# Kernel tuning notes

Measured on AMD Instinct MI355X. Metric: run time of the kernel, lower is better.

## Reference

```python
import jax, jax.numpy as jnp
import numpy as np

EPS = 1e-08
ORDINAL = 2.0

def setup_inputs() -> dict:
    key = jax.random.key(0)
    k1, k2, k3, k4, k5 = jax.random.split(key, 5)
    B, IN, OUT = 1024, 256, 1024
    inputs = jax.random.normal(k1, (B, IN), dtype=jnp.float32)
    weights = jax.random.normal(k2, (OUT, IN), dtype=jnp.float32) * (1.0 / np.sqrt(IN))
    biases = jax.random.normal(k3, (OUT,), dtype=jnp.float32) * (1.0 / np.sqrt(IN))
    centers = jax.random.normal(k4, (OUT, IN), dtype=jnp.float32) * 0.1
    # diag inv covars ~ U(3/(IN+0.5), 3/(IN-0.5)) per reset_parameters
    inv_covars = jax.random.uniform(k5, (OUT, IN), dtype=jnp.float32,
                                    minval=3.0 / (IN + 0.5), maxval=3.0 / (IN - 0.5))
    return {"inputs": inputs, "weights": weights, "biases": biases,
            "centers": centers, "inv_covars": inv_covars}

def reference(inputs, weights, biases, centers, inv_covars):
    # linear part: [B, OUT]
    l = inputs @ weights.T + biases
    # diag covar path (ordinal = 2.0, so the 1e-32 stabilizer is absent and
    # pow(c^2, 1/ordinal) == |c| after clamping):
    # g[b, z] = sum_i ( |x[b,i] - c[z,i]| * sqrt(clamp(ic[z,i])^2) )^2
    ic = jnp.minimum(inv_covars, 1.0 / EPS)
    scale = jnp.power(ic * ic, 1.0 / ORDINAL)  # [OUT, IN]
    diff = jnp.abs(inputs[:, None, :] - centers[None, :, :]) * scale[None, :, :]  # [B, OUT, IN]
    g = jnp.exp(-jnp.sum(jnp.power(diff, ORDINAL), axis=-1))  # [B, OUT]
    res = l * g
    return (res, g)
```

## Files before the change

kernel.cpp:

```cpp
#include <hip/hip_runtime.h>
#include <hip/hip_bf16.h>
#include <math.h>


typedef __attribute__((ext_vector_type(8))) short short8;
typedef __attribute__((ext_vector_type(4))) float floatx4;

#define MFMA __builtin_amdgcn_mfma_f32_16x16x32_bf16
#define INDIM 256
#define OUTD  1024
#define BD    1024
#define TM 32
#define TN 32
#define TK 64
#define KSTR 72

__device__ __forceinline__ unsigned pkbf(float a, float b) {
    union { __hip_bfloat162 h; unsigned u; } v;
    v.h = __float22bfloat162_rn(make_float2(a, b));
    return v.u;
}

__global__ __launch_bounds__(256)
void fgn_fused(const float* __restrict__ X, const float* __restrict__ W,
               const float* __restrict__ Bias, const float* __restrict__ C,
               const float* __restrict__ IC, float* __restrict__ Out)
{
    __shared__ __align__(16) unsigned short As [TM * KSTR];
    __shared__ __align__(16) unsigned short As2[TM * KSTR];
    __shared__ __align__(16) unsigned short Bw [TN * KSTR];
    __shared__ __align__(16) unsigned short Bg1[TN * KSTR];
    __shared__ __align__(16) unsigned short Bg2[TN * KSTR];
    __shared__ float sCz[TN];

    const int b    = blockIdx.x;
    const int xcd  = b & 7;
    const int n0   = (xcd + 8 * ((b >> 3) & 3)) * TN;
    const int m0   = (b >> 5) * TM;

    const int t    = threadIdx.x;
    const int w    = t >> 6;
    const int lane = t & 63;
    const int r    = lane & 15;
    const int q    = lane >> 4;
    const int mt   = w & 1;
    const int nt   = w >> 1;

    const int srow = t >> 3;
    const int sk   = (t & 7) << 3;

    floatx4 zero = {0.f, 0.f, 0.f, 0.f};
    floatx4 accL = zero;
    floatx4 accG = zero;
    float czp = 0.f;

    for (int k0 = 0; k0 < INDIM; k0 += TK) {
        const float4* xp = (const float4*)&X[(size_t)(m0 + srow) * INDIM + k0 + sk];
        float4 x0 = xp[0], x1 = xp[1];
        const size_t bo = (size_t)(n0 + srow) * INDIM + k0 + sk;
        const float4* wp = (const float4*)&W[bo];
        const float4* cp = (const float4*)&C[bo];
        const float4* ip = (const float4*)&IC[bo];
        float4 w0 = wp[0], w1 = wp[1];
        float4 c0 = cp[0], c1 = cp[1];
        float4 i0 = ip[0], i1 = ip[1];

        __syncthreads();

        {
            float xf[8] = {x0.x,x0.y,x0.z,x0.w, x1.x,x1.y,x1.z,x1.w};
            uint4* pa  = (uint4*)&As [srow * KSTR + sk];
            uint4* pa2 = (uint4*)&As2[srow * KSTR + sk];
            pa[0]  = make_uint4(pkbf(xf[0],xf[1]), pkbf(xf[2],xf[3]),
                                pkbf(xf[4],xf[5]), pkbf(xf[6],xf[7]));
            pa2[0] = make_uint4(pkbf(xf[0]*xf[0],xf[1]*xf[1]), pkbf(xf[2]*xf[2],xf[3]*xf[3]),
                                pkbf(xf[4]*xf[4],xf[5]*xf[5]), pkbf(xf[6]*xf[6],xf[7]*xf[7]));
        }
        {
            float wf[8] = {w0.x,w0.y,w0.z,w0.w, w1.x,w1.y,w1.z,w1.w};
            float cf[8] = {c0.x,c0.y,c0.z,c0.w, c1.x,c1.y,c1.z,c1.w};
            float ff[8] = {i0.x,i0.y,i0.z,i0.w, i1.x,i1.y,i1.z,i1.w};
            float g1[8], g2[8];
            #pragma unroll
            for (int e = 0; e < 8; ++e) {
                float s  = fminf(ff[e], 1e8f);
                float qq = s * s;
                g2[e] = qq;
                g1[e] = -2.f * cf[e] * qq;
                czp  = fmaf(cf[e] * cf[e], qq, czp);
            }
            const int bb = srow * KSTR + sk;
            *(uint4*)&Bw [bb] = make_uint4(pkbf(wf[0],wf[1]), pkbf(wf[2],wf[3]),
                                           pkbf(wf[4],wf[5]), pkbf(wf[6],wf[7]));
            *(uint4*)&Bg1[bb] = make_uint4(pkbf(g1[0],g1[1]), pkbf(g1[2],g1[3]),
                                           pkbf(g1[4],g1[5]), pkbf(g1[6],g1[7]));
            *(uint4*)&Bg2[bb] = make_uint4(pkbf(g2[0],g2[1]), pkbf(g2[2],g2[3]),
                                           pkbf(g2[4],g2[5]), pkbf(g2[6],g2[7]));
        }
        if (k0 + TK >= INDIM) {
            czp += __shfl_down(czp, 4);
            czp += __shfl_down(czp, 2);
            czp += __shfl_down(czp, 1);
            if ((t & 7) == 0) sCz[srow] = czp;
        }
        __syncthreads();

        #pragma unroll
        for (int kk = 0; kk < 2; ++kk) {
            const int ko = kk * 32 + q * 8;
            short8 a0  = *(const short8*)&As [(mt * 16 + r) * KSTR + ko];
            short8 a2  = *(const short8*)&As2[(mt * 16 + r) * KSTR + ko];
            const int br = (nt * 16 + r) * KSTR + ko;
            short8 bwf = *(const short8*)&Bw [br];
            short8 b1f = *(const short8*)&Bg1[br];
            short8 b2f = *(const short8*)&Bg2[br];
            accL = MFMA(a0, bwf, accL, 0, 0, 0);
            accG = MFMA(a0, b1f, accG, 0, 0, 0);
            accG = MFMA(a2, b2f, accG, 0, 0, 0);
        }
    }

    float* OutR = Out;
    float* OutG = Out + (size_t)BD * OUTD;
    const int n      = n0 + nt * 16 + r;
    const float bias = Bias[n];
    const float cz   = sCz[nt * 16 + r];
    #pragma unroll
    for (int reg = 0; reg < 4; ++reg) {
        const int m = m0 + mt * 16 + q * 4 + reg;
        const float g   = expf(-(accG[reg] + cz));
        const float res = (accL[reg] + bias) * g;
        OutR[(size_t)m * OUTD + n] = res;
        OutG[(size_t)m * OUTD + n] = g;
    }
}

extern "C" void kernel_launch(void* const* d_in, const int* in_sizes, int n_in,
                              void* d_out, int out_size, void* d_ws, size_t ws_size,
                              hipStream_t stream) {
    const float* X    = (const float*)d_in[0];
    const float* W    = (const float*)d_in[1];
    const float* Bias = (const float*)d_in[2];
    const float* C    = (const float*)d_in[3];
    const float* IC   = (const float*)d_in[4];
    float* Out = (float*)d_out;

    fgn_fused<<<1024, 256, 0, stream>>>(X, W, Bias, C, IC, Out);
}
```

Baseline: 71.22 us.

## Split preprocessing into prep kernel and double-buffer bf16 tiles via direct global-to-LDS loads

A separate prep kernel now converts X, X², W and the Gaussian factors to bf16 and precomputes the per-output constant term once, instead of every tile block redoing that conversion. The main kernel streams those bf16 operands straight into XOR-swizzled LDS with global_load_lds, double-buffered so the next K tile loads while the current one computes. It also uses 64-row M tiles with 512 threads. The cost is a second kernel launch, a workspace round trip, and less occupancy from the larger blocks.

```diff
diff --git a/kernel.cpp b/kernel.cpp
--- a/kernel.cpp
+++ b/kernel.cpp
@@ -7,13 +7,10 @@
 typedef __attribute__((ext_vector_type(4))) float floatx4;
 
 #define MFMA __builtin_amdgcn_mfma_f32_16x16x32_bf16
-#define INDIM 256
-#define OUTD  1024
-#define BD    1024
-#define TM 32
-#define TN 32
-#define TK 64
-#define KSTR 72
+
+#define GLDS16(g, l) __builtin_amdgcn_global_load_lds(                      \
+    (const __attribute__((address_space(1))) void*)(g),                     \
+    (__attribute__((address_space(3))) void*)(l), 16, 0, 0)
 
 __device__ __forceinline__ unsigned pkbf(float a, float b) {
     union { __hip_bfloat162 h; unsigned u; } v;
@@ -22,116 +19,139 @@
 }
 
 __global__ __launch_bounds__(256)
-void fgn_fused(const float* __restrict__ X, const float* __restrict__ W,
-               const float* __restrict__ Bias, const float* __restrict__ C,
-               const float* __restrict__ IC, float* __restrict__ Out)
+void fgn_prep(const float* __restrict__ X, const float* __restrict__ W,
+              const float* __restrict__ C, const float* __restrict__ IC,
+              unsigned short* __restrict__ XB, unsigned short* __restrict__ X2B,
+              unsigned short* __restrict__ WB, unsigned short* __restrict__ G1,
+              unsigned short* __restrict__ G2, float* __restrict__ CZ)
 {
-    __shared__ __align__(16) unsigned short As [TM * KSTR];
-    __shared__ __align__(16) unsigned short As2[TM * KSTR];
-    __shared__ __align__(16) unsigned short Bw [TN * KSTR];
-    __shared__ __align__(16) unsigned short Bg1[TN * KSTR];
-    __shared__ __align__(16) unsigned short Bg2[TN * KSTR];
-    __shared__ float sCz[TN];
+    const int t = threadIdx.x, w = t >> 6, l = t & 63;
+    const int b = blockIdx.x;
+    if (b < 256) {
+        const int z = b * 4 + w;
+        const int o = z * 256 + l * 4;
+        const float4 c4 = *(const float4*)&C[o];
+        const float4 i4 = *(const float4*)&IC[o];
+        const float4 w4 = *(const float4*)&W[o];
+        float s;
+        s = fminf(i4.x, 1e8f); const float q0 = s * s;
+        s = fminf(i4.y, 1e8f); const float q1 = s * s;
+        s = fminf(i4.z, 1e8f); const float q2 = s * s;
+        s = fminf(i4.w, 1e8f); const float q3 = s * s;
+        float czp = c4.x*c4.x*q0 + c4.y*c4.y*q1 + c4.z*c4.z*q2 + c4.w*c4.w*q3;
+        *(uint2*)&WB[o] = make_uint2(pkbf(w4.x, w4.y), pkbf(w4.z, w4.w));
+        *(uint2*)&G1[o] = make_uint2(pkbf(-2.f*c4.x*q0, -2.f*c4.y*q1),
+                                     pkbf(-2.f*c4.z*q2, -2.f*c4.w*q3));
+        *(uint2*)&G2[o] = make_uint2(pkbf(q0, q1), pkbf(q2, q3));
+        #pragma unroll
+        for (int off = 32; off; off >>= 1) czp += __shfl_down(czp, off);
+        if (l == 0) CZ[z] = czp;
+    } else {
+        const int m = (b - 256) * 4 + w;
+        const int o = m * 256 + l * 4;
+        const float4 x4 = *(const float4*)&X[o];
+        *(uint2*)&XB[o]  = make_uint2(pkbf(x4.x, x4.y), pkbf(x4.z, x4.w));
+        *(uint2*)&X2B[o] = make_uint2(pkbf(x4.x*x4.x, x4.y*x4.y),
+                                      pkbf(x4.z*x4.z, x4.w*x4.w));
+    }
+}
 
-    const int b    = blockIdx.x;
-    const int xcd  = b & 7;
-    const int n0   = (xcd + 8 * ((b >> 3) & 3)) * TN;
-    const int m0   = (b >> 5) * TM;
+#define L_AX   0
+#define L_AX2  8192
+#define L_BW   16384
+#define L_BG1  20480
+#define L_BG2  24576
+#define L_BUF  28672
+
+__global__ __launch_bounds__(512)
+void fgn_main(const unsigned short* __restrict__ XB, const unsigned short* __restrict__ X2B,
+              const unsigned short* __restrict__ WB, const unsigned short* __restrict__ G1,
+              const unsigned short* __restrict__ G2, const float* __restrict__ Bias,
+              const float* __restrict__ CZ, float* __restrict__ Out)
+{
+    __shared__ __align__(16) char lds[2 * L_BUF];
+
+    const int b  = blockIdx.x;
+    const int n0 = ((b & 7) + 8 * ((b >> 3) & 3)) * 32;
+    const int m0 = (b >> 5) * 64;
 
     const int t    = threadIdx.x;
     const int w    = t >> 6;
     const int lane = t & 63;
     const int r    = lane & 15;
     const int q    = lane >> 4;
-    const int mt   = w & 1;
-    const int nt   = w >> 1;
+    const int mt   = w & 3;
+    const int nt   = w >> 2;
 
-    const int srow = t >> 3;
-    const int sk   = (t & 7) << 3;
+    const int rt = t >> 3;
+    const int cs = ((t & 7) << 4) ^ ((rt & 7) << 4);
+    const int srcA = (m0 + rt) * 512 + cs;
+    const int srcB = (n0 + rt) * 512 + cs;
+    const int wbase = (t >> 6) << 10;
 
     floatx4 zero = {0.f, 0.f, 0.f, 0.f};
     floatx4 accL = zero;
     floatx4 accG = zero;
-    float czp = 0.f;
 
-    for (int k0 = 0; k0 < INDIM; k0 += TK) {
-        const float4* xp = (const float4*)&X[(size_t)(m0 + srow) * INDIM + k0 + sk];
-        float4 x0 = xp[0], x1 = xp[1];
-        const size_t bo = (size_t)(n0 + srow) * INDIM + k0 + sk;
-        const float4* wp = (const float4*)&W[bo];
-        const float4* cp = (const float4*)&C[bo];
-        const float4* ip = (const float4*)&IC[bo];
-        float4 w0 = wp[0], w1 = wp[1];
-        float4 c0 = cp[0], c1 = cp[1];
-        float4 i0 = ip[0], i1 = ip[1];
+    auto STAGE = [&](int buf, int k0) {
+        char* L = lds + buf * L_BUF;
+        const int kb = k0 << 1;
+        GLDS16((const char*)XB  + srcA + kb, L + L_AX  + wbase);
+        GLDS16((const char*)X2B + srcA + kb, L + L_AX2 + wbase);
+        if (t < 256) {
+            GLDS16((const char*)WB + srcB + kb, L + L_BW  + wbase);
+            GLDS16((const char*)G1 + srcB + kb, L + L_BG1 + wbase);
+            GLDS16((const char*)G2 + srcB + kb, L + L_BG2 + wbase);
+        }
+    };
 
-        __syncthreads();
-
-        {
-            float xf[8] = {x0.x,x0.y,x0.z,x0.w, x1.x,x1.y,x1.z,x1.w};
-            uint4* pa  = (uint4*)&As [srow * KSTR + sk];
-            uint4* pa2 = (uint4*)&As2[srow * KSTR + sk];
-            pa[0]  = make_uint4(pkbf(xf[0],xf[1]), pkbf(xf[2],xf[3]),
-                                pkbf(xf[4],xf[5]), pkbf(xf[6],xf[7]));
-            pa2[0] = make_uint4(pkbf(xf[0]*xf[0],xf[1]*xf[1]), pkbf(xf[2]*xf[2],xf[3]*xf[3]),
-                                pkbf(xf[4]*xf[4],xf[5]*xf[5]), pkbf(xf[6]*xf[6],xf[7]*xf[7]));
-        }
-        {
-            float wf[8] = {w0.x,w0.y,w0.z,w0.w, w1.x,w1.y,w1.z,w1.w};
-            float cf[8] = {c0.x,c0.y,c0.z,c0.w, c1.x,c1.y,c1.z,c1.w};
-            float ff[8] = {i0.x,i0.y,i0.z,i0.w, i1.x,i1.y,i1.z,i1.w};
-            float g1[8], g2[8];
-            #pragma unroll
-            for (int e = 0; e < 8; ++e) {
-                float s  = fminf(ff[e], 1e8f);
-                float qq = s * s;
-                g2[e] = qq;
-                g1[e] = -2.f * cf[e] * qq;
-                czp  = fmaf(cf[e] * cf[e], qq, czp);
-            }
-            const int bb = srow * KSTR + sk;
-            *(uint4*)&Bw [bb] = make_uint4(pkbf(wf[0],wf[1]), pkbf(wf[2],wf[3]),
-                                           pkbf(wf[4],wf[5]), pkbf(wf[6],wf[7]));
-            *(uint4*)&Bg1[bb] = make_uint4(pkbf(g1[0],g1[1]), pkbf(g1[2],g1[3]),
-                                           pkbf(g1[4],g1[5]), pkbf(g1[6],g1[7]));
-            *(uint4*)&Bg2[bb] = make_uint4(pkbf(g2[0],g2[1]), pkbf(g2[2],g2[3]),
-                                           pkbf(g2[4],g2[5]), pkbf(g2[6],g2[7]));
-        }
-        if (k0 + TK >= INDIM) {
-            czp += __shfl_down(czp, 4);
-            czp += __shfl_down(czp, 2);
-            czp += __shfl_down(czp, 1);
-            if ((t & 7) == 0) sCz[srow] = czp;
-        }
-        __syncthreads();
-
+    const int arow = mt * 16 + r;
+    const int brow = nt * 16 + r;
+    auto COMPUTE = [&](int buf) {
+        const char* L = lds + buf * L_BUF;
         #pragma unroll
         for (int kk = 0; kk < 2; ++kk) {
-            const int ko = kk * 32 + q * 8;
-            short8 a0  = *(const short8*)&As [(mt * 16 + r) * KSTR + ko];
-            short8 a2  = *(const short8*)&As2[(mt * 16 + r) * KSTR + ko];
-            const int br = (nt * 16 + r) * KSTR + ko;
-            short8 bwf = *(const short8*)&Bw [br];
-            short8 b1f = *(const short8*)&Bg1[br];
-            short8 b2f = *(const short8*)&Bg2[br];
-            accL = MFMA(a0, bwf, accL, 0, 0, 0);
-            accG = MFMA(a0, b1f, accG, 0, 0, 0);
-            accG = MFMA(a2, b2f, accG, 0, 0, 0);
+            const int ca = kk * 64 + q * 16;
+            const int ao = arow * 128 + (ca ^ ((arow & 7) << 4));
+            const int bo = brow * 128 + (ca ^ ((brow & 7) << 4));
+            short8 a0 = *(const short8*)(L + L_AX  + ao);
+            short8 a2 = *(const short8*)(L + L_AX2 + ao);
+            short8 bw = *(const short8*)(L + L_BW  + bo);
+            short8 b1 = *(const short8*)(L + L_BG1 + bo);
+            short8 b2 = *(const short8*)(L + L_BG2 + bo);
+            accL = MFMA(a0, bw, accL, 0, 0, 0);
+            accG = MFMA(a0, b1, accG, 0, 0, 0);
+            accG = MFMA(a2, b2, accG, 0, 0, 0);
+        }
+    };
+
+    STAGE(0, 0);
+    asm volatile("s_waitcnt vmcnt(0)" ::: "memory");
+    __syncthreads();
+
+    int cur = 0;
+    #pragma unroll
+    for (int k0 = 0; k0 < 256; k0 += 64) {
+        if (k0 + 64 < 256) STAGE(cur ^ 1, k0 + 64);
+        COMPUTE(cur);
+        if (k0 + 64 < 256) {
+            asm volatile("s_waitcnt vmcnt(0)" ::: "memory");
+            __syncthreads();
+            cur ^= 1;
         }
     }
 
-    float* OutR = Out;
-    float* OutG = Out + (size_t)BD * OUTD;
-    const int n      = n0 + nt * 16 + r;
+    const int   n    = n0 + nt * 16 + r;
     const float bias = Bias[n];
-    const float cz   = sCz[nt * 16 + r];
+    const float cz   = CZ[n];
+    float* OutG = Out + (size_t)1024 * 1024;
     #pragma unroll
     for (int reg = 0; reg < 4; ++reg) {
         const int m = m0 + mt * 16 + q * 4 + reg;
         const float g   = expf(-(accG[reg] + cz));
         const float res = (accL[reg] + bias) * g;
-        OutR[(size_t)m * OUTD + n] = res;
-        OutG[(size_t)m * OUTD + n] = g;
+        Out [(size_t)m * 1024 + n] = res;
+        OutG[(size_t)m * 1024 + n] = g;
     }
 }
 
@@ -145,5 +165,13 @@
     const float* IC   = (const float*)d_in[4];
     float* Out = (float*)d_out;
 
-    fgn_fused<<<1024, 256, 0, stream>>>(X, W, Bias, C, IC, Out);
+    unsigned short* XB  = (unsigned short*)d_ws;
+    unsigned short* X2B = XB  + 262144;
+    unsigned short* WB  = X2B + 262144;
+    unsigned short* G1  = WB  + 262144;
+    unsigned short* G2  = G1  + 262144;
+    float*          CZ  = (float*)(G2 + 262144);
+
+    fgn_prep<<<512, 256, 0, stream>>>(X, W, C, IC, XB, X2B, WB, G1, G2, CZ);
+    fgn_main<<<512, 512, 0, stream>>>(XB, X2B, WB, G1, G2, Bias, CZ, Out);
 }
```

New measurement: 70.65 us. About the same (-0.8%).

## Enlarge tiles to 128x32 with 512 threads and prefetch next K slice

Applied to the files above, without the earlier changes.

Each block now covers 128 rows by 32 columns with 512 threads, and each wave computes two 16x16 output tiles. This reuses the B-side operands (W, centers, inverse covariances) across four times as many rows, which cuts redundant global loads and the repeated conversion work on those operands. Half the threads load W while the other half load C and IC. Global loads for the next K slice are issued before the MFMA compute of the current one, so memory latency overlaps with compute. The grid shrinks to 256 blocks, which lowers the number of blocks per CU and drops the previous XCD-aware block mapping.

```diff
diff --git a/kernel.cpp b/kernel.cpp
--- a/kernel.cpp
+++ b/kernel.cpp
@@ -7,12 +7,6 @@
 typedef __attribute__((ext_vector_type(4))) float floatx4;
 
 #define MFMA __builtin_amdgcn_mfma_f32_16x16x32_bf16
-#define INDIM 256
-#define OUTD  1024
-#define BD    1024
-#define TM 32
-#define TN 32
-#define TK 64
 #define KSTR 72
 
 __device__ __forceinline__ unsigned pkbf(float a, float b) {
@@ -21,63 +15,84 @@
     return v.u;
 }
 
-__global__ __launch_bounds__(256)
-void fgn_fused(const float* __restrict__ X, const float* __restrict__ W,
-               const float* __restrict__ Bias, const float* __restrict__ C,
-               const float* __restrict__ IC, float* __restrict__ Out)
+__global__ __launch_bounds__(512)
+void fgn_one(const float* __restrict__ X, const float* __restrict__ W,
+             const float* __restrict__ Bias, const float* __restrict__ C,
+             const float* __restrict__ IC, float* __restrict__ Out)
 {
-    __shared__ __align__(16) unsigned short As [TM * KSTR];
-    __shared__ __align__(16) unsigned short As2[TM * KSTR];
-    __shared__ __align__(16) unsigned short Bw [TN * KSTR];
-    __shared__ __align__(16) unsigned short Bg1[TN * KSTR];
-    __shared__ __align__(16) unsigned short Bg2[TN * KSTR];
-    __shared__ float sCz[TN];
+    __shared__ __align__(16) unsigned short As [128 * KSTR];
+    __shared__ __align__(16) unsigned short As2[128 * KSTR];
+    __shared__ __align__(16) unsigned short Bw [32 * KSTR];
+    __shared__ __align__(16) unsigned short Bg1[32 * KSTR];
+    __shared__ __align__(16) unsigned short Bg2[32 * KSTR];
+    __shared__ float sCz[32];
 
-    const int b    = blockIdx.x;
-    const int xcd  = b & 7;
-    const int n0   = (xcd + 8 * ((b >> 3) & 3)) * TN;
-    const int m0   = (b >> 5) * TM;
+    const int b  = blockIdx.x;
+    const int m0 = (b & 7) * 128;
+    const int n0 = (b >> 3) * 32;
 
     const int t    = threadIdx.x;
     const int w    = t >> 6;
     const int lane = t & 63;
     const int r    = lane & 15;
     const int q    = lane >> 4;
-    const int mt   = w & 1;
-    const int nt   = w >> 1;
+    const int mt   = w & 3;
+    const int nt   = w >> 2;
 
-    const int srow = t >> 3;
-    const int sk   = (t & 7) << 3;
+    const int arow = t >> 3;
+    const int ach  = (t & 7) << 3;
+    const bool isW = (t < 256);
+    const int brow = (t & 255) >> 3;
+
+    float4 xa0, xa1, xb0, xb1;
+    float4 w0, w1, c0, c1, i0, i1;
+    float czp = 0.f;
 
     floatx4 zero = {0.f, 0.f, 0.f, 0.f};
-    floatx4 accL = zero;
-    floatx4 accG = zero;
-    float czp = 0.f;
+    floatx4 accL0 = zero, accL1 = zero, accG0 = zero, accG1 = zero;
 
-    for (int k0 = 0; k0 < INDIM; k0 += TK) {
-        const float4* xp = (const float4*)&X[(size_t)(m0 + srow) * INDIM + k0 + sk];
-        float4 x0 = xp[0], x1 = xp[1];
-        const size_t bo = (size_t)(n0 + srow) * INDIM + k0 + sk;
-        const float4* wp = (const float4*)&W[bo];
-        const float4* cp = (const float4*)&C[bo];
-        const float4* ip = (const float4*)&IC[bo];
-        float4 w0 = wp[0], w1 = wp[1];
-        float4 c0 = cp[0], c1 = cp[1];
-        float4 i0 = ip[0], i1 = ip[1];
+    auto LOADS = [&](int k0) {
+        const float4* p;
+        p = (const float4*)&X[(size_t)(m0 + arow) * 256 + k0 + ach];
+        xa0 = p[0]; xa1 = p[1];
+        p = (const float4*)&X[(size_t)(m0 + arow + 64) * 256 + k0 + ach];
+        xb0 = p[0]; xb1 = p[1];
+        if (isW) {
+            p = (const float4*)&W[(size_t)(n0 + brow) * 256 + k0 + ach];
+            w0 = p[0]; w1 = p[1];
+        } else {
+            p = (const float4*)&C[(size_t)(n0 + brow) * 256 + k0 + ach];
+            c0 = p[0]; c1 = p[1];
+            p = (const float4*)&IC[(size_t)(n0 + brow) * 256 + k0 + ach];
+            i0 = p[0]; i1 = p[1];
+        }
+    };
 
-        __syncthreads();
-
+    auto STORE_LDS = [&](bool last) {
         {
-            float xf[8] = {x0.x,x0.y,x0.z,x0.w, x1.x,x1.y,x1.z,x1.w};
-            uint4* pa  = (uint4*)&As [srow * KSTR + sk];
-            uint4* pa2 = (uint4*)&As2[srow * KSTR + sk];
-            pa[0]  = make_uint4(pkbf(xf[0],xf[1]), pkbf(xf[2],xf[3]),
-                                pkbf(xf[4],xf[5]), pkbf(xf[6],xf[7]));
-            pa2[0] = make_uint4(pkbf(xf[0]*xf[0],xf[1]*xf[1]), pkbf(xf[2]*xf[2],xf[3]*xf[3]),
-                                pkbf(xf[4]*xf[4],xf[5]*xf[5]), pkbf(xf[6]*xf[6],xf[7]*xf[7]));
+            float f0[8] = {xa0.x,xa0.y,xa0.z,xa0.w, xa1.x,xa1.y,xa1.z,xa1.w};
+            float f1[8] = {xb0.x,xb0.y,xb0.z,xb0.w, xb1.x,xb1.y,xb1.z,xb1.w};
+            const int a0 = arow * KSTR + ach;
+            const int a1 = (arow + 64) * KSTR + ach;
+            *(uint4*)&As [a0] = make_uint4(pkbf(f0[0],f0[1]), pkbf(f0[2],f0[3]),
+                                           pkbf(f0[4],f0[5]), pkbf(f0[6],f0[7]));
+            *(uint4*)&As2[a0] = make_uint4(pkbf(f0[0]*f0[0],f0[1]*f0[1]),
+                                           pkbf(f0[2]*f0[2],f0[3]*f0[3]),
+                                           pkbf(f0[4]*f0[4],f0[5]*f0[5]),
+                                           pkbf(f0[6]*f0[6],f0[7]*f0[7]));
+            *(uint4*)&As [a1] = make_uint4(pkbf(f1[0],f1[1]), pkbf(f1[2],f1[3]),
+                                           pkbf(f1[4],f1[5]), pkbf(f1[6],f1[7]));
+            *(uint4*)&As2[a1] = make_uint4(pkbf(f1[0]*f1[0],f1[1]*f1[1]),
+                                           pkbf(f1[2]*f1[2],f1[3]*f1[3]),
+                                           pkbf(f1[4]*f1[4],f1[5]*f1[5]),
+                                           pkbf(f1[6]*f1[6],f1[7]*f1[7]));
         }
-        {
-            float wf[8] = {w0.x,w0.y,w0.z,w0.w, w1.x,w1.y,w1.z,w1.w};
+        const int bb = brow * KSTR + ach;
+        if (isW) {
+            float f[8] = {w0.x,w0.y,w0.z,w0.w, w1.x,w1.y,w1.z,w1.w};
+            *(uint4*)&Bw[bb] = make_uint4(pkbf(f[0],f[1]), pkbf(f[2],f[3]),
+                                          pkbf(f[4],f[5]), pkbf(f[6],f[7]));
+        } else {
             float cf[8] = {c0.x,c0.y,c0.z,c0.w, c1.x,c1.y,c1.z,c1.w};
             float ff[8] = {i0.x,i0.y,i0.z,i0.w, i1.x,i1.y,i1.z,i1.w};
             float g1[8], g2[8];
@@ -89,49 +104,66 @@
                 g1[e] = -2.f * cf[e] * qq;
                 czp  = fmaf(cf[e] * cf[e], qq, czp);
             }
-            const int bb = srow * KSTR + sk;
-            *(uint4*)&Bw [bb] = make_uint4(pkbf(wf[0],wf[1]), pkbf(wf[2],wf[3]),
-                                           pkbf(wf[4],wf[5]), pkbf(wf[6],wf[7]));
             *(uint4*)&Bg1[bb] = make_uint4(pkbf(g1[0],g1[1]), pkbf(g1[2],g1[3]),
                                            pkbf(g1[4],g1[5]), pkbf(g1[6],g1[7]));
             *(uint4*)&Bg2[bb] = make_uint4(pkbf(g2[0],g2[1]), pkbf(g2[2],g2[3]),
                                            pkbf(g2[4],g2[5]), pkbf(g2[6],g2[7]));
+            if (last) {
+                czp += __shfl_down(czp, 4);
+                czp += __shfl_down(czp, 2);
+                czp += __shfl_down(czp, 1);
+                if ((t & 7) == 0) sCz[brow] = czp;
+            }
         }
-        if (k0 + TK >= INDIM) {
-            czp += __shfl_down(czp, 4);
-            czp += __shfl_down(czp, 2);
-            czp += __shfl_down(czp, 1);
-            if ((t & 7) == 0) sCz[srow] = czp;
-        }
-        __syncthreads();
+    };
 
+    const int ar0 = (mt * 32 + r) * KSTR;
+    const int ar1 = ar0 + 16 * KSTR;
+    const int br  = (nt * 16 + r) * KSTR;
+    auto COMPUTE = [&]() {
         #pragma unroll
         for (int kk = 0; kk < 2; ++kk) {
             const int ko = kk * 32 + q * 8;
-            short8 a0  = *(const short8*)&As [(mt * 16 + r) * KSTR + ko];
-            short8 a2  = *(const short8*)&As2[(mt * 16 + r) * KSTR + ko];
-            const int br = (nt * 16 + r) * KSTR + ko;
-            short8 bwf = *(const short8*)&Bw [br];
-            short8 b1f = *(const short8*)&Bg1[br];
-            short8 b2f = *(const short8*)&Bg2[br];
-            accL = MFMA(a0, bwf, accL, 0, 0, 0);
-            accG = MFMA(a0, b1f, accG, 0, 0, 0);
-            accG = MFMA(a2, b2f, accG, 0, 0, 0);
+            short8 a00 = *(const short8*)&As [ar0 + ko];
+            short8 a01 = *(const short8*)&As [ar1 + ko];
+            short8 a20 = *(const short8*)&As2[ar0 + ko];
+            short8 a21 = *(const short8*)&As2[ar1 + ko];
+            short8 bwf = *(const short8*)&Bw [br + ko];
+            short8 b1f = *(const short8*)&Bg1[br + ko];
+            short8 b2f = *(const short8*)&Bg2[br + ko];
+            accL0 = MFMA(a00, bwf, accL0, 0, 0, 0);
+            accL1 = MFMA(a01, bwf, accL1, 0, 0, 0);
+            accG0 = MFMA(a00, b1f, accG0, 0, 0, 0);
+            accG1 = MFMA(a01, b1f, accG1, 0, 0, 0);
+            accG0 = MFMA(a20, b2f, accG0, 0, 0, 0);
+            accG1 = MFMA(a21, b2f, accG1, 0, 0, 0);
         }
+    };
+
+    LOADS(0);
+    #pragma unroll
+    for (int k0 = 0; k0 < 256; k0 += 64) {
+        __syncthreads();
+        STORE_LDS(k0 == 192);
+        __syncthreads();
+        if (k0 < 192) LOADS(k0 + 64);
+        COMPUTE();
     }
 
-    float* OutR = Out;
-    float* OutG = Out + (size_t)BD * OUTD;
-    const int n      = n0 + nt * 16 + r;
+    const int   n    = n0 + nt * 16 + r;
     const float bias = Bias[n];
     const float cz   = sCz[nt * 16 + r];
+    float* OutG = Out + (size_t)1024 * 1024;
     #pragma unroll
     for (int reg = 0; reg < 4; ++reg) {
-        const int m = m0 + mt * 16 + q * 4 + reg;
-        const float g   = expf(-(accG[reg] + cz));
-        const float res = (accL[reg] + bias) * g;
-        OutR[(size_t)m * OUTD + n] = res;
-        OutG[(size_t)m * OUTD + n] = g;
+        const int ma = m0 + mt * 32 + q * 4 + reg;
+        const float ga   = expf(-(accG0[reg] + cz));
+        Out [(size_t)ma * 1024 + n] = (accL0[reg] + bias) * ga;
+        OutG[(size_t)ma * 1024 + n] = ga;
+        const int mb = ma + 16;
+        const float gb   = expf(-(accG1[reg] + cz));
+        Out [(size_t)mb * 1024 + n] = (accL1[reg] + bias) * gb;
+        OutG[(size_t)mb * 1024 + n] = gb;
     }
 }
 
@@ -145,5 +177,5 @@
     const float* IC   = (const float*)d_in[4];
     float* Out = (float*)d_out;
 
-    fgn_fused<<<1024, 256, 0, stream>>>(X, W, Bias, C, IC, Out);
+    fgn_one<<<256, 512, 0, stream>>>(X, W, Bias, C, IC, Out);
 }
```

After: 76.31 us. 7.1% more time.
